# Performance work log

Measured on AMD Instinct MI355X. Metric: run time of the kernel, lower is better.

## Reference

```python
import jax, jax.numpy as jnp
import numpy as np

DEPTH = 4  # truncation depth of the tensor algebra


def _tprod(a, b):
    # tensor (outer) product of level-i and level-j terms, flattened row-major
    # a: (B, C^i), b: (B, C^j) -> (B, C^(i+j))
    return (a[:, :, None] * b[:, None, :]).reshape(a.shape[0], -1)


def _exp_levels(dx):
    # exp(dx) in the truncated tensor algebra: level k = dx^{\otimes k} / k!
    levels = [dx]
    for k in range(2, DEPTH + 1):
        levels.append(_tprod(levels[-1], dx) / k)
    return tuple(levels)


def _chen(a, b):
    # Chen's identity: (a \otimes b)_k = a_k + b_k + sum_{i=1}^{k-1} a_i \otimes b_{k-i}
    out = []
    for k in range(1, DEPTH + 1):
        t = a[k - 1] + b[k - 1]
        for i in range(1, k):
            t = t + _tprod(a[i - 1], b[k - 1 - i])
        out.append(t)
    return tuple(out)


def _log_levels(s):
    # log(1 + x) = sum_{n>=1} (-1)^{n+1}/n x^{\otimes n}, x = S - 1 (levels 1..DEPTH)
    res = list(s)
    power = [t for t in s]  # x^{\otimes 1}; entries may become None (structurally zero)
    for n in range(2, DEPTH + 1):
        new = [None] * DEPTH
        for k in range(n, DEPTH + 1):
            acc = None
            for i in range(n - 1, k):
                if power[i - 1] is None:
                    continue
                term = _tprod(power[i - 1], s[k - i - 1])
                acc = term if acc is None else acc + term
            new[k - 1] = acc
        power = new
        coef = ((-1.0) ** (n + 1)) / n
        for k in range(n, DEPTH + 1):
            if power[k - 1] is not None:
                res[k - 1] = res[k - 1] + coef * power[k - 1]
    return tuple(res)


def _logsignature(path):
    # path: (B, L, C); no basepoint, stream=False, inverse=False, mode='expand'
    dxs = jnp.moveaxis(path[:, 1:] - path[:, :-1], 1, 0)  # (L-1, B, C)
    init = _exp_levels(dxs[0])

    def step(carry, dx):
        return _chen(carry, _exp_levels(dx)), None

    sig, _ = jax.lax.scan(step, init, dxs[1:])
    logsig = _log_levels(sig)
    return jnp.concatenate(logsig, axis=-1)  # (B, C + C^2 + ... + C^DEPTH)


def setup_inputs() -> dict:
    key = jax.random.key(0)
    # scale so high tensor-algebra levels stay well-conditioned in fp32
    path = 0.1 * jax.random.normal(key, (64, 256, 16), dtype=jnp.float32)
    return {"path": path}


def reference(path):
    return _logsignature(path)
```

## Files before the change

kernel.cpp:

```cpp
#include <hip/hip_runtime.h>


#define NC 16
#define NL 256
#define NB 64
#define OUTB 69904
#define SIG123 4368
#define OFF_L2 16
#define OFF_L3 272
#define OFF_L4 4368
#define LCS 260

#define SIGA_OFF 0
#define SIGB_OFF (NB * SIG123)

typedef float v2f __attribute__((ext_vector_type(2)));

__global__ __launch_bounds__(128, 2) void k_scan(const float* __restrict__ path,
                                                 float* __restrict__ out,
                                                 float* __restrict__ sigA,
                                                 float* __restrict__ sigB) {
    const int bid = blockIdx.x;
    const int j = bid >> 4;
    const int a = bid & 15;
    const int tid = threadIdx.x;
    const int h = tid >> 6;
    const int b = (tid >> 2) & 15;
    const int c0 = tid & 3;

    __shared__ float Lp[NL * NC];
    __shared__ float Lc[NC * LCS];

    const float* pj = path + (size_t)j * NL * NC;
#pragma unroll
    for (int k = 0; k < 8; ++k) {
        const int f = tid + k * 128;
        *(float4*)&Lp[f * 4] = *(const float4*)&pj[f * 4];
    }
    __syncthreads();

    float4 dif[8];
#pragma unroll
    for (int k = 0; k < 8; ++k) {
        const int f = tid + k * 128;
        if (f < 1020) {
            const float4 x0 = *(const float4*)&Lp[f * 4];
            const float4 x1 = *(const float4*)&Lp[f * 4 + 16];
            dif[k] = make_float4(x1.x - x0.x, x1.y - x0.y, x1.z - x0.z, x1.w - x0.w);
        } else {
            dif[k] = make_float4(0.f, 0.f, 0.f, 0.f);
        }
    }
    __syncthreads();
#pragma unroll
    for (int k = 0; k < 8; ++k) {
        const int f = tid + k * 128;
        *(float4*)&Lp[f * 4] = dif[k];
        const int t = f >> 2;
        const int i0 = 4 * (f & 3);
        Lc[(i0 + 0) * LCS + t] = dif[k].x;
        Lc[(i0 + 1) * LCS + t] = dif[k].y;
        Lc[(i0 + 2) * LCS + t] = dif[k].z;
        Lc[(i0 + 3) * LCS + t] = dif[k].w;
    }
    __syncthreads();

    v2f s4q[4][8];
#pragma unroll
    for (int m = 0; m < 4; ++m)
#pragma unroll
        for (int d = 0; d < 8; ++d) s4q[m][d] = (v2f){0.f, 0.f};
    float s3q[4] = {0.f, 0.f, 0.f, 0.f};
    float s2ab = 0.f, s1a = 0.f;

    auto body = [&](const float4& q0, const float4& q1, const float4& q2,
                    const float4& q3, float dxa, float dxb, float dc0, float dc1,
                    float dc2, float dc3) {
        const float P = dxb * s1a;
        const float Q = dxb * dxa;
        const float pre4 = fmaf(1.f / 6.f, P, fmaf(1.f / 24.f, Q, 0.5f * s2ab));
        const float U = fmaf(0.5f, P, fmaf(1.f / 6.f, Q, s2ab));
        const float T0 = fmaf(dc0, pre4, s3q[0]);
        const float T1 = fmaf(dc1, pre4, s3q[1]);
        const float T2 = fmaf(dc2, pre4, s3q[2]);
        const float T3 = fmaf(dc3, pre4, s3q[3]);
        const v2f dv2[8] = {{q0.x, q0.y}, {q0.z, q0.w}, {q1.x, q1.y}, {q1.z, q1.w},
                            {q2.x, q2.y}, {q2.z, q2.w}, {q3.x, q3.y}, {q3.z, q3.w}};
        const v2f Tv0 = {T0, T0}, Tv1 = {T1, T1}, Tv2 = {T2, T2}, Tv3 = {T3, T3};
#pragma unroll
        for (int d = 0; d < 8; ++d) {
            s4q[0][d] = __builtin_elementwise_fma(dv2[d], Tv0, s4q[0][d]);
            s4q[1][d] = __builtin_elementwise_fma(dv2[d], Tv1, s4q[1][d]);
            s4q[2][d] = __builtin_elementwise_fma(dv2[d], Tv2, s4q[2][d]);
            s4q[3][d] = __builtin_elementwise_fma(dv2[d], Tv3, s4q[3][d]);
        }
        s3q[0] = fmaf(dc0, U, s3q[0]);
        s3q[1] = fmaf(dc1, U, s3q[1]);
        s3q[2] = fmaf(dc2, U, s3q[2]);
        s3q[3] = fmaf(dc3, U, s3q[3]);
        s2ab = fmaf(dxb, fmaf(0.5f, dxa, s1a), s2ab);
        s1a += dxa;
    };

    int t = h * 128;
    for (int it = 0; it < 32; ++it, t += 4) {
        const float4 va = *(const float4*)(Lc + a * LCS + t);
        const float4 vb = *(const float4*)(Lc + b * LCS + t);
        const float4 vc0 = *(const float4*)(Lc + c0 * LCS + t);
        const float4 vc1 = *(const float4*)(Lc + (c0 + 4) * LCS + t);
        const float4 vc2 = *(const float4*)(Lc + (c0 + 8) * LCS + t);
        const float4 vc3 = *(const float4*)(Lc + (c0 + 12) * LCS + t);
#pragma unroll
        for (int u = 0; u < 4; ++u) {
            const float* r = Lp + (t + u) * NC;
            const float4 q0 = *(const float4*)(r);
            const float4 q1 = *(const float4*)(r + 4);
            const float4 q2 = *(const float4*)(r + 8);
            const float4 q3 = *(const float4*)(r + 12);
            const float dxa = (u == 0) ? va.x : (u == 1) ? va.y : (u == 2) ? va.z : va.w;
            const float dxb = (u == 0) ? vb.x : (u == 1) ? vb.y : (u == 2) ? vb.z : vb.w;
            const float d0 = (u == 0) ? vc0.x : (u == 1) ? vc0.y : (u == 2) ? vc0.z : vc0.w;
            const float d1 = (u == 0) ? vc1.x : (u == 1) ? vc1.y : (u == 2) ? vc1.z : vc1.w;
            const float d2 = (u == 0) ? vc2.x : (u == 1) ? vc2.y : (u == 2) ? vc2.z : vc2.w;
            const float d3 = (u == 0) ? vc3.x : (u == 1) ? vc3.y : (u == 2) ? vc3.z : vc3.w;
            body(q0, q1, q2, q3, dxa, dxb, d0, d1, d2, d3);
        }
    }

    __syncthreads();
    float* sl = Lc + (size_t)(b * 4 + c0) * 65;
    if (h == 0) {
#pragma unroll
        for (int m = 0; m < 4; ++m)
#pragma unroll
            for (int q = 0; q < 4; ++q)
                *(float4*)&sl[m * 16 + q * 4] =
                    make_float4(s4q[m][2 * q].x, s4q[m][2 * q].y,
                                s4q[m][2 * q + 1].x, s4q[m][2 * q + 1].y);
    }
    __syncthreads();
    if (h == 1) {
#pragma unroll
        for (int m = 0; m < 4; ++m)
#pragma unroll
            for (int q = 0; q < 4; ++q) {
                float4 v = *(const float4*)&sl[m * 16 + q * 4];
                v.x += s4q[m][2 * q].x;
                v.y += s4q[m][2 * q].y;
                v.z += s4q[m][2 * q + 1].x;
                v.w += s4q[m][2 * q + 1].y;
                *(float4*)&sl[m * 16 + q * 4] = v;
            }
    }
    __syncthreads();
    {
        float* o4 = out + (size_t)j * OUTB + OFF_L4 + a * 4096;
#pragma unroll
        for (int k = 0; k < 8; ++k) {
            const int f = tid + k * 128;
            const int m0 = f * 4;
            const int bb = m0 >> 8;
            const int cc = (m0 >> 4) & 15;
            const int dd = m0 & 15;
            const int src = (bb * 4 + (cc & 3)) * 65 + (cc >> 2) * 16 + dd;
            *(float4*)(o4 + m0) = *(const float4*)&Lc[src];
        }
    }

    float* sg = (h ? sigB : sigA) + (size_t)j * SIG123;
#pragma unroll
    for (int m = 0; m < 4; ++m)
        sg[OFF_L3 + (a * 16 + b) * 16 + c0 + 4 * m] = s3q[m];
    if (c0 == 0) sg[OFF_L2 + a * 16 + b] = s2ab;
    if ((tid & 63) == 0) sg[a] = s1a;
}

__global__ __launch_bounds__(256) void k_log(const float* __restrict__ sigA,
                                             const float* __restrict__ sigB,
                                             float* __restrict__ out) {
    const int bid = blockIdx.x;
    const int j = bid >> 4;
    const int a = bid & 15;
    const int tid = threadIdx.x;
    const int q = tid >> 4;
    const int r = tid & 15;

    const float* A = sigA + (size_t)j * SIG123;
    const float* Bp = sigB + (size_t)j * SIG123;

    __shared__ float S1m[16], B1s[16], A2s[16];
    __shared__ float S2m[256], B2s[256], A3s[256];
    __shared__ float S3m[4096];

    const float b1r = Bp[r];
    const float b2t = Bp[OFF_L2 + tid];

    if (tid < 16) {
        const float bb = Bp[tid];
        B1s[tid] = bb;
        S1m[tid] = A[tid] + bb;
        A2s[tid] = A[OFF_L2 + a * 16 + tid];
    }
    B2s[tid] = b2t;
    S2m[tid] = A[OFF_L2 + tid] + b2t + A[q] * b1r;
    A3s[tid] = A[OFF_L3 + a * 256 + tid];
#pragma unroll
    for (int k = 0; k < 16; ++k) {
        const int m = k * 256 + tid;
        S3m[m] = A[OFF_L3 + m] + Bp[OFF_L3 + m] + A[k] * b2t + A[OFF_L2 + k * 16 + q] * b1r;
    }
    __syncthreads();

    const float s1a = S1m[a];
    const float A1a = A[a];
    float* outj = out + (size_t)j * OUTB;
    float* o4 = outj + OFF_L4 + a * 4096;
    const float Ac = -0.5f * s1a;

#pragma unroll
    for (int k = 0; k < 4; ++k) {
        const int f = tid + k * 256;
        const int m0 = f * 4;
        const int bb = m0 >> 8;
        const int cc = (m0 >> 4) & 15;
        const float s1b = S1m[bb], s1c = S1m[cc];
        const float s2ab = S2m[a * 16 + bb];
        const float s2bc = S2m[bb * 16 + cc];
        const float s3abc = S3m[a * 256 + (m0 >> 4)];
        const float a3x = A3s[m0 >> 4];
        const float a2x = A2s[bb];

        const float4 a4 = *(const float4*)(o4 + m0);
        const float4 b3v = *(const float4*)(Bp + OFF_L3 + m0);
        const float4 b2v = *(const float4*)(&B2s[m0 & 255]);
        const float4 b1v = *(const float4*)(&B1s[m0 & 15]);
        const float4 v3 = *(const float4*)(&S3m[m0]);
        const float4 v2 = *(const float4*)(&S2m[m0 & 255]);
        const float4 v1 = *(const float4*)(&S1m[m0 & 15]);

        const float Bv = fmaf((1.f / 3.f) * s1a, s1b, -0.5f * s2ab);
        const float Cv = -0.5f * s3abc + (1.f / 3.f) * fmaf(s1a, s2bc, s2ab * s1c)
                         - 0.25f * s1a * s1b * s1c;
        float4 rv;
        rv.x = a4.x + fmaf(A1a, b3v.x, fmaf(a2x, b2v.x, a3x * b1v.x));
        rv.y = a4.y + fmaf(A1a, b3v.y, fmaf(a2x, b2v.y, a3x * b1v.y));
        rv.z = a4.z + fmaf(A1a, b3v.z, fmaf(a2x, b2v.z, a3x * b1v.z));
        rv.w = a4.w + fmaf(A1a, b3v.w, fmaf(a2x, b2v.w, a3x * b1v.w));
        rv.x = fmaf(Ac, v3.x, rv.x) + fmaf(Bv, v2.x, Cv * v1.x);
        rv.y = fmaf(Ac, v3.y, rv.y) + fmaf(Bv, v2.y, Cv * v1.y);
        rv.z = fmaf(Ac, v3.z, rv.z) + fmaf(Bv, v2.z, Cv * v1.z);
        rv.w = fmaf(Ac, v3.w, rv.w) + fmaf(Bv, v2.w, Cv * v1.w);
        *(float4*)(o4 + m0) = rv;
    }

    {
        const float s1b = S1m[q], s1c = S1m[r];
        const float s2ab = S2m[a * 16 + q];
        const float s2bc = S2m[q * 16 + r];
        const float s3abc = S3m[a * 256 + tid];
        const float r3 = s3abc - 0.5f * fmaf(s1a, s2bc, s2ab * s1c)
                         + (1.f / 3.f) * s1a * s1b * s1c;
        outj[OFF_L3 + a * 256 + tid] = r3;
    }
    if (tid < 16) outj[OFF_L2 + a * 16 + tid] = fmaf(-0.5f * s1a, S1m[tid], S2m[a * 16 + tid]);
    if (tid == 0) outj[a] = s1a;
}

extern "C" void kernel_launch(void* const* d_in, const int* in_sizes, int n_in,
                              void* d_out, int out_size, void* d_ws, size_t ws_size,
                              hipStream_t stream) {
    const float* path = (const float*)d_in[0];
    float* out = (float*)d_out;
    float* ws = (float*)d_ws;
    float* sigA = ws + SIGA_OFF;
    float* sigB = ws + SIGB_OFF;

    k_scan<<<NB * 16, 128, 0, stream>>>(path, out, sigA, sigB);
    k_log<<<NB * 16, 256, 0, stream>>>(sigA, sigB, out);
}
```

Before: 106.5 us.

## Compute two level-1 indices per scan block and double-buffer LDS loads

Each k_scan block now handles two 'a' indices (a0 and a0+8), so it runs half as many blocks. Each block reuses the Lp row loads and the b/c operand loads across both accumulator sets, which halves the redundant path loading and LDS traffic per FMA. The time loop is unrolled by two, with ping-pong register buffers that prefetch the next group's LDS values. Register use roughly doubles, so launch bounds drop to one block per CU, and the grid of 512 blocks may leave parts of the GPU underused.

```diff
diff --git a/kernel.cpp b/kernel.cpp
--- a/kernel.cpp
+++ b/kernel.cpp
@@ -16,13 +16,43 @@
 
 typedef float v2f __attribute__((ext_vector_type(2)));
 
-__global__ __launch_bounds__(128, 2) void k_scan(const float* __restrict__ path,
+#define EXTRACT(V, U) ((U) == 0 ? (V).x : (U) == 1 ? (V).y : (U) == 2 ? (V).z : (V).w)
+
+#define STEPA(S4, S3, S2, S1, DXA, DXB, D0, D1, D2, D3, Q0, Q1, Q2, Q3)          \
+    {                                                                            \
+        const float P_ = (DXB) * (S1);                                           \
+        const float Q_ = (DXB) * (DXA);                                          \
+        const float pre4_ = fmaf(1.f / 6.f, P_, fmaf(1.f / 24.f, Q_, 0.5f * (S2))); \
+        const float U_ = fmaf(0.5f, P_, fmaf(1.f / 6.f, Q_, (S2)));              \
+        const float T0_ = fmaf((D0), pre4_, (S3)[0]);                            \
+        const float T1_ = fmaf((D1), pre4_, (S3)[1]);                            \
+        const float T2_ = fmaf((D2), pre4_, (S3)[2]);                            \
+        const float T3_ = fmaf((D3), pre4_, (S3)[3]);                            \
+        const v2f dv2_[8] = {{Q0.x, Q0.y}, {Q0.z, Q0.w}, {Q1.x, Q1.y}, {Q1.z, Q1.w}, \
+                             {Q2.x, Q2.y}, {Q2.z, Q2.w}, {Q3.x, Q3.y}, {Q3.z, Q3.w}}; \
+        const v2f Tv0_ = {T0_, T0_}, Tv1_ = {T1_, T1_}, Tv2_ = {T2_, T2_},       \
+                  Tv3_ = {T3_, T3_};                                             \
+        _Pragma("unroll") for (int d_ = 0; d_ < 8; ++d_) {                       \
+            S4[0][d_] = __builtin_elementwise_fma(dv2_[d_], Tv0_, S4[0][d_]);    \
+            S4[1][d_] = __builtin_elementwise_fma(dv2_[d_], Tv1_, S4[1][d_]);    \
+            S4[2][d_] = __builtin_elementwise_fma(dv2_[d_], Tv2_, S4[2][d_]);    \
+            S4[3][d_] = __builtin_elementwise_fma(dv2_[d_], Tv3_, S4[3][d_]);    \
+        }                                                                        \
+        (S3)[0] = fmaf((D0), U_, (S3)[0]);                                       \
+        (S3)[1] = fmaf((D1), U_, (S3)[1]);                                       \
+        (S3)[2] = fmaf((D2), U_, (S3)[2]);                                       \
+        (S3)[3] = fmaf((D3), U_, (S3)[3]);                                       \
+        (S2) = fmaf((DXB), fmaf(0.5f, (DXA), (S1)), (S2));                       \
+        (S1) += (DXA);                                                           \
+    }
+
+__global__ __launch_bounds__(128, 1) void k_scan(const float* __restrict__ path,
                                                  float* __restrict__ out,
                                                  float* __restrict__ sigA,
                                                  float* __restrict__ sigB) {
     const int bid = blockIdx.x;
-    const int j = bid >> 4;
-    const int a = bid & 15;
+    const int j = bid >> 3;
+    const int a0 = bid & 7;
     const int tid = threadIdx.x;
     const int h = tid >> 6;
     const int b = (tid >> 2) & 15;
@@ -65,114 +95,115 @@
     }
     __syncthreads();
 
-    v2f s4q[4][8];
+    v2f s4A[4][8], s4B[4][8];
 #pragma unroll
     for (int m = 0; m < 4; ++m)
 #pragma unroll
-        for (int d = 0; d < 8; ++d) s4q[m][d] = (v2f){0.f, 0.f};
-    float s3q[4] = {0.f, 0.f, 0.f, 0.f};
-    float s2ab = 0.f, s1a = 0.f;
-
-    auto body = [&](const float4& q0, const float4& q1, const float4& q2,
-                    const float4& q3, float dxa, float dxb, float dc0, float dc1,
-                    float dc2, float dc3) {
-        const float P = dxb * s1a;
-        const float Q = dxb * dxa;
-        const float pre4 = fmaf(1.f / 6.f, P, fmaf(1.f / 24.f, Q, 0.5f * s2ab));
-        const float U = fmaf(0.5f, P, fmaf(1.f / 6.f, Q, s2ab));
-        const float T0 = fmaf(dc0, pre4, s3q[0]);
-        const float T1 = fmaf(dc1, pre4, s3q[1]);
-        const float T2 = fmaf(dc2, pre4, s3q[2]);
-        const float T3 = fmaf(dc3, pre4, s3q[3]);
-        const v2f dv2[8] = {{q0.x, q0.y}, {q0.z, q0.w}, {q1.x, q1.y}, {q1.z, q1.w},
-                            {q2.x, q2.y}, {q2.z, q2.w}, {q3.x, q3.y}, {q3.z, q3.w}};
-        const v2f Tv0 = {T0, T0}, Tv1 = {T1, T1}, Tv2 = {T2, T2}, Tv3 = {T3, T3};
-#pragma unroll
         for (int d = 0; d < 8; ++d) {
-            s4q[0][d] = __builtin_elementwise_fma(dv2[d], Tv0, s4q[0][d]);
-            s4q[1][d] = __builtin_elementwise_fma(dv2[d], Tv1, s4q[1][d]);
-            s4q[2][d] = __builtin_elementwise_fma(dv2[d], Tv2, s4q[2][d]);
-            s4q[3][d] = __builtin_elementwise_fma(dv2[d], Tv3, s4q[3][d]);
+            s4A[m][d] = (v2f){0.f, 0.f};
+            s4B[m][d] = (v2f){0.f, 0.f};
         }
-        s3q[0] = fmaf(dc0, U, s3q[0]);
-        s3q[1] = fmaf(dc1, U, s3q[1]);
-        s3q[2] = fmaf(dc2, U, s3q[2]);
-        s3q[3] = fmaf(dc3, U, s3q[3]);
-        s2ab = fmaf(dxb, fmaf(0.5f, dxa, s1a), s2ab);
-        s1a += dxa;
-    };
+    float s3qA[4] = {0.f, 0.f, 0.f, 0.f};
+    float s3qB[4] = {0.f, 0.f, 0.f, 0.f};
+    float s2abA = 0.f, s2abB = 0.f, s1aA = 0.f, s1aB = 0.f;
+
+#define LOADG(VA0, VA1, VB, VC0, VC1, VC2, VC3, TT)              \
+    VA0 = *(const float4*)(Lc + a0 * LCS + (TT));                \
+    VA1 = *(const float4*)(Lc + (a0 + 8) * LCS + (TT));          \
+    VB = *(const float4*)(Lc + b * LCS + (TT));                  \
+    VC0 = *(const float4*)(Lc + c0 * LCS + (TT));                \
+    VC1 = *(const float4*)(Lc + (c0 + 4) * LCS + (TT));          \
+    VC2 = *(const float4*)(Lc + (c0 + 8) * LCS + (TT));          \
+    VC3 = *(const float4*)(Lc + (c0 + 12) * LCS + (TT));
+
+#define COMP4(VA0, VA1, VB, VC0, VC1, VC2, VC3, TT)                              \
+    _Pragma("unroll") for (int u_ = 0; u_ < 4; ++u_) {                           \
+        const float* rr_ = Lp + ((TT) + u_) * NC;                                \
+        const float4 q0_ = *(const float4*)(rr_);                                \
+        const float4 q1_ = *(const float4*)(rr_ + 4);                            \
+        const float4 q2_ = *(const float4*)(rr_ + 8);                            \
+        const float4 q3_ = *(const float4*)(rr_ + 12);                           \
+        const float dxa0_ = EXTRACT(VA0, u_), dxa1_ = EXTRACT(VA1, u_);          \
+        const float dxb_ = EXTRACT(VB, u_);                                      \
+        const float d0_ = EXTRACT(VC0, u_), d1_ = EXTRACT(VC1, u_);              \
+        const float d2_ = EXTRACT(VC2, u_), d3_ = EXTRACT(VC3, u_);              \
+        STEPA(s4A, s3qA, s2abA, s1aA, dxa0_, dxb_, d0_, d1_, d2_, d3_, q0_, q1_, \
+              q2_, q3_)                                                          \
+        STEPA(s4B, s3qB, s2abB, s1aB, dxa1_, dxb_, d0_, d1_, d2_, d3_, q0_, q1_, \
+              q2_, q3_)                                                          \
+    }
 
     int t = h * 128;
-    for (int it = 0; it < 32; ++it, t += 4) {
-        const float4 va = *(const float4*)(Lc + a * LCS + t);
-        const float4 vb = *(const float4*)(Lc + b * LCS + t);
-        const float4 vc0 = *(const float4*)(Lc + c0 * LCS + t);
-        const float4 vc1 = *(const float4*)(Lc + (c0 + 4) * LCS + t);
-        const float4 vc2 = *(const float4*)(Lc + (c0 + 8) * LCS + t);
-        const float4 vc3 = *(const float4*)(Lc + (c0 + 12) * LCS + t);
-#pragma unroll
-        for (int u = 0; u < 4; ++u) {
-            const float* r = Lp + (t + u) * NC;
-            const float4 q0 = *(const float4*)(r);
-            const float4 q1 = *(const float4*)(r + 4);
-            const float4 q2 = *(const float4*)(r + 8);
-            const float4 q3 = *(const float4*)(r + 12);
-            const float dxa = (u == 0) ? va.x : (u == 1) ? va.y : (u == 2) ? va.z : va.w;
-            const float dxb = (u == 0) ? vb.x : (u == 1) ? vb.y : (u == 2) ? vb.z : vb.w;
-            const float d0 = (u == 0) ? vc0.x : (u == 1) ? vc0.y : (u == 2) ? vc0.z : vc0.w;
-            const float d1 = (u == 0) ? vc1.x : (u == 1) ? vc1.y : (u == 2) ? vc1.z : vc1.w;
-            const float d2 = (u == 0) ? vc2.x : (u == 1) ? vc2.y : (u == 2) ? vc2.z : vc2.w;
-            const float d3 = (u == 0) ? vc3.x : (u == 1) ? vc3.y : (u == 2) ? vc3.z : vc3.w;
-            body(q0, q1, q2, q3, dxa, dxb, d0, d1, d2, d3);
-        }
-    }
-
-    __syncthreads();
-    float* sl = Lc + (size_t)(b * 4 + c0) * 65;
-    if (h == 0) {
-#pragma unroll
-        for (int m = 0; m < 4; ++m)
-#pragma unroll
-            for (int q = 0; q < 4; ++q)
-                *(float4*)&sl[m * 16 + q * 4] =
-                    make_float4(s4q[m][2 * q].x, s4q[m][2 * q].y,
-                                s4q[m][2 * q + 1].x, s4q[m][2 * q + 1].y);
-    }
-    __syncthreads();
-    if (h == 1) {
-#pragma unroll
-        for (int m = 0; m < 4; ++m)
-#pragma unroll
-            for (int q = 0; q < 4; ++q) {
-                float4 v = *(const float4*)&sl[m * 16 + q * 4];
-                v.x += s4q[m][2 * q].x;
-                v.y += s4q[m][2 * q].y;
-                v.z += s4q[m][2 * q + 1].x;
-                v.w += s4q[m][2 * q + 1].y;
-                *(float4*)&sl[m * 16 + q * 4] = v;
-            }
-    }
-    __syncthreads();
-    {
-        float* o4 = out + (size_t)j * OUTB + OFF_L4 + a * 4096;
-#pragma unroll
-        for (int k = 0; k < 8; ++k) {
-            const int f = tid + k * 128;
-            const int m0 = f * 4;
-            const int bb = m0 >> 8;
-            const int cc = (m0 >> 4) & 15;
-            const int dd = m0 & 15;
-            const int src = (bb * 4 + (cc & 3)) * 65 + (cc >> 2) * 16 + dd;
-            *(float4*)(o4 + m0) = *(const float4*)&Lc[src];
-        }
-    }
+    float4 Aa0, Aa1, Ab, Ac0, Ac1, Ac2, Ac3;
+    float4 Ba0, Ba1, Bb, Bc0, Bc1, Bc2, Bc3;
+    LOADG(Aa0, Aa1, Ab, Ac0, Ac1, Ac2, Ac3, t)
+    for (int it = 0; it < 16; ++it, t += 8) {
+        LOADG(Ba0, Ba1, Bb, Bc0, Bc1, Bc2, Bc3, t + 4)
+        COMP4(Aa0, Aa1, Ab, Ac0, Ac1, Ac2, Ac3, t)
+        LOADG(Aa0, Aa1, Ab, Ac0, Ac1, Ac2, Ac3, t + 8)
+        COMP4(Ba0, Ba1, Bb, Bc0, Bc1, Bc2, Bc3, t + 4)
+    }
+#undef LOADG
+#undef COMP4
+
+    __syncthreads();
+
+#define EPI(S4X, AV)                                                             \
+    {                                                                            \
+        float* sl_ = Lc + (size_t)(b * 4 + c0) * 65;                             \
+        if (h == 0) {                                                            \
+            _Pragma("unroll") for (int m_ = 0; m_ < 4; ++m_)                     \
+                _Pragma("unroll") for (int q_ = 0; q_ < 4; ++q_)                 \
+                    *(float4*)&sl_[m_ * 16 + q_ * 4] = make_float4(              \
+                        S4X[m_][2 * q_].x, S4X[m_][2 * q_].y,                    \
+                        S4X[m_][2 * q_ + 1].x, S4X[m_][2 * q_ + 1].y);           \
+        }                                                                        \
+        __syncthreads();                                                         \
+        if (h == 1) {                                                            \
+            _Pragma("unroll") for (int m_ = 0; m_ < 4; ++m_)                     \
+                _Pragma("unroll") for (int q_ = 0; q_ < 4; ++q_) {               \
+                    float4 v_ = *(const float4*)&sl_[m_ * 16 + q_ * 4];          \
+                    v_.x += S4X[m_][2 * q_].x;                                   \
+                    v_.y += S4X[m_][2 * q_].y;                                   \
+                    v_.z += S4X[m_][2 * q_ + 1].x;                               \
+                    v_.w += S4X[m_][2 * q_ + 1].y;                               \
+                    *(float4*)&sl_[m_ * 16 + q_ * 4] = v_;                       \
+                }                                                                \
+        }                                                                        \
+        __syncthreads();                                                         \
+        {                                                                        \
+            float* o4_ = out + (size_t)j * OUTB + OFF_L4 + (AV) * 4096;          \
+            _Pragma("unroll") for (int k_ = 0; k_ < 8; ++k_) {                   \
+                const int f_ = tid + k_ * 128;                                   \
+                const int m0_ = f_ * 4;                                          \
+                const int bb_ = m0_ >> 8;                                        \
+                const int cc_ = (m0_ >> 4) & 15;                                 \
+                const int dd_ = m0_ & 15;                                        \
+                const int src_ = (bb_ * 4 + (cc_ & 3)) * 65 + (cc_ >> 2) * 16 + dd_; \
+                *(float4*)(o4_ + m0_) = *(const float4*)&Lc[src_];               \
+            }                                                                    \
+        }                                                                        \
+        __syncthreads();                                                         \
+    }
+
+    EPI(s4A, a0)
+    EPI(s4B, a0 + 8)
+#undef EPI
 
     float* sg = (h ? sigB : sigA) + (size_t)j * SIG123;
 #pragma unroll
-    for (int m = 0; m < 4; ++m)
-        sg[OFF_L3 + (a * 16 + b) * 16 + c0 + 4 * m] = s3q[m];
-    if (c0 == 0) sg[OFF_L2 + a * 16 + b] = s2ab;
-    if ((tid & 63) == 0) sg[a] = s1a;
+    for (int m = 0; m < 4; ++m) {
+        sg[OFF_L3 + (a0 * 16 + b) * 16 + c0 + 4 * m] = s3qA[m];
+        sg[OFF_L3 + ((a0 + 8) * 16 + b) * 16 + c0 + 4 * m] = s3qB[m];
+    }
+    if (c0 == 0) {
+        sg[OFF_L2 + a0 * 16 + b] = s2abA;
+        sg[OFF_L2 + (a0 + 8) * 16 + b] = s2abB;
+    }
+    if ((tid & 63) == 0) {
+        sg[a0] = s1aA;
+        sg[a0 + 8] = s1aB;
+    }
 }
 
 __global__ __launch_bounds__(256) void k_log(const float* __restrict__ sigA,
@@ -275,6 +306,6 @@
     float* sigA = ws + SIGA_OFF;
     float* sigB = ws + SIGB_OFF;
 
-    k_scan<<<NB * 16, 128, 0, stream>>>(path, out, sigA, sigB);
+    k_scan<<<NB * 8, 128, 0, stream>>>(path, out, sigA, sigB);
     k_log<<<NB * 16, 256, 0, stream>>>(sigA, sigB, out);
 }
```

Result: slower. 112.9 us (+6.1%).
